# Performance work log

Hardware: AMD Instinct MI355X
Metric: run time of the kernel (lower is better)

Reference implementation:

```python
import jax, jax.numpy as jnp
import numpy as np

H = 768
R = 24


def setup_inputs() -> dict:
    key = jax.random.key(0)
    ks = jax.random.split(key, 9)
    B, S = 4, 256
    hidden = jax.random.normal(ks[0], (B, S, H), dtype=jnp.float32)
    # ConcatHandshaking fc: Linear(2H -> H); torch weight shape (out,in)=(H,2H)
    fc_w = jax.random.normal(ks[1], (H, 2 * H), dtype=jnp.float32) * (1.0 / np.sqrt(2 * H))
    fc_b = jnp.zeros((H,), dtype=jnp.float32)
    # h2t: Linear(H -> 2)
    h2t_w = jax.random.normal(ks[2], (2, H), dtype=jnp.float32) * (1.0 / np.sqrt(H))
    h2t_b = jnp.zeros((2,), dtype=jnp.float32)
    # h2h / t2t TaggingProjector: R independent Linear(H -> 3), batched as (R,3,H)
    h2h_w = jax.random.normal(ks[3], (R, 3, H), dtype=jnp.float32) * (1.0 / np.sqrt(H))
    h2h_b = jnp.zeros((R, 3), dtype=jnp.float32)
    t2t_w = jax.random.normal(ks[4], (R, 3, H), dtype=jnp.float32) * (1.0 / np.sqrt(H))
    t2t_b = jnp.zeros((R, 3), dtype=jnp.float32)
    return {
        "hidden": hidden,
        "fc_w": fc_w, "fc_b": fc_b,
        "h2t_w": h2t_w, "h2t_b": h2t_b,
        "h2h_w": h2h_w, "h2h_b": h2h_b,
        "t2t_w": t2t_w, "t2t_b": t2t_b,
    }


def _handshaking(hidden, fc_w, fc_b):
    # hidden: (B, S, H). Pairs (i, j) with i <= j in row-major (torch loop) order.
    S = hidden.shape[1]
    idx_i, idx_j = jnp.triu_indices(S)  # each (P,), P = S(S+1)/2
    # concat([h_i, h_j]) @ W^T == h_i @ Wl^T + h_j @ Wr^T  (avoids (B,P,2H) buffer)
    Wl = fc_w[:, :H]  # (H, H)
    Wr = fc_w[:, H:]  # (H, H)
    left = jnp.einsum('bsh,oh->bso', hidden, Wl)   # (B, S, H)
    right = jnp.einsum('bsh,oh->bso', hidden, Wr)  # (B, S, H)
    hs = jnp.tanh(left[:, idx_i, :] + right[:, idx_j, :] + fc_b)  # (B, P, H)
    return hs


def reference(hidden, fc_w, fc_b, h2t_w, h2t_b, h2h_w, h2h_b, t2t_w, t2t_b):
    hs = _handshaking(hidden, fc_w, fc_b)  # (B, P, H)
    # h2t: plain Linear(H->2), logits (no softmax in original)
    h2t = jnp.einsum('bph,oh->bpo', hs, h2t_w) + h2t_b  # (B, P, 2)
    # TaggingProjector: batched per-relation Linear(H->3), then softmax over tags
    h2h = jax.nn.softmax(jnp.einsum('bph,rth->brpt', hs, h2h_w) + h2h_b[None, :, None, :], axis=-1)
    t2t = jax.nn.softmax(jnp.einsum('bph,rth->brpt', hs, t2t_w) + t2t_b[None, :, None, :], axis=-1)
    return (h2t, h2h, t2t)
```

## Files before the change

kernel.cpp:

```cpp
#include <hip/hip_runtime.h>
#include <hip/hip_bf16.h>

#define H 768
#define SEQ 256
#define NPAIR 32896
#define NOUTP 160
#define OFF_H2H 263168u
#define OFF_T2T 9737216u

#define N_BPK 122880
#define N_FCW 1179648
#define SCL 2.8853900817779268f

typedef short bf16x8 __attribute__((ext_vector_type(8)));
typedef float f32x4 __attribute__((ext_vector_type(4)));

__device__ __forceinline__ float tanh_s(float xs) {
    float e = __builtin_amdgcn_exp2f(xs);
    return fmaf(-2.0f, __builtin_amdgcn_rcpf(e + 1.0f), 1.0f);
}
__device__ __forceinline__ float bf_lo(int w){ return __uint_as_float(((unsigned)w) << 16); }
__device__ __forceinline__ float bf_hi(int w){ return __uint_as_float(((unsigned)w) & 0xffff0000u); }
__device__ __forceinline__ float bfu(unsigned short u){ return __uint_as_float(((unsigned)u) << 16); }
__device__ __forceinline__ int cvtpk(float lo, float hi) {
    int r;
    asm("v_cvt_pk_bf16_f32 %0, %1, %2" : "=v"(r) : "v"(lo), "v"(hi));
    return r;
}
__device__ __forceinline__ unsigned short bf16r(float x){
    unsigned int u = __float_as_uint(x);
    u += 0x7fffu + ((u >> 16) & 1u);
    return (unsigned short)(u >> 16);
}
__device__ __forceinline__ bf16x8 tanh_frag(int4 lv, int4 rv) {
    int4 st;
    st.x = cvtpk(tanh_s(bf_lo(lv.x) + bf_lo(rv.x)), tanh_s(bf_hi(lv.x) + bf_hi(rv.x)));
    st.y = cvtpk(tanh_s(bf_lo(lv.y) + bf_lo(rv.y)), tanh_s(bf_hi(lv.y) + bf_hi(rv.y)));
    st.z = cvtpk(tanh_s(bf_lo(lv.z) + bf_lo(rv.z)), tanh_s(bf_hi(lv.z) + bf_hi(rv.z)));
    st.w = cvtpk(tanh_s(bf_lo(lv.w) + bf_lo(rv.w)), tanh_s(bf_hi(lv.w) + bf_hi(rv.w)));
    return __builtin_bit_cast(bf16x8, st);
}

typedef const __attribute__((address_space(1))) unsigned int* as1_u32p;
typedef __attribute__((address_space(3))) unsigned int* as3_u32p;
__device__ __forceinline__ void gload_lds16(const void* g, void* l) {
    __builtin_amdgcn_global_load_lds((as1_u32p)g, (as3_u32p)l, 16, 0, 0);
}

__device__ __forceinline__ int row_start(int i) { return i * SEQ - (i * (i - 1)) / 2; }
__device__ __forceinline__ void pair_ij(int p, int& oi, int& oj) {
    double disc = 263169.0 - 8.0 * (double)p;
    int i = (int)((513.0 - sqrt(disc)) * 0.5);
    if (i > 0 && row_start(i) > p) --i;
    while (row_start(i + 1) <= p) ++i;
    oi = i;
    oj = i + (p - row_start(i));
}

__global__ __launch_bounds__(256) void pack_kernel(
    const float* __restrict__ h2t_w, const float* __restrict__ h2h_w,
    const float* __restrict__ t2t_w, const float* __restrict__ h2t_b,
    const float* __restrict__ h2h_b, const float* __restrict__ t2t_b,
    const float* __restrict__ fc_w,
    unsigned short* __restrict__ Bpk, unsigned short* __restrict__ fcwb,
    float* __restrict__ bc)
{
    int idx = blockIdx.x * 256 + threadIdx.x;
    if (idx < N_BPK) {
        int j = idx & 7, lane = (idx >> 3) & 63, rest = idx >> 9;
        int f = rest % 10, k32 = rest / 10;
        int n = f * 16 + (lane & 15);
        int k = k32 * 32 + ((lane >> 4) << 3) + j;
        float v = 0.f;
        if (n < 2)        v = h2t_w[n * H + k];
        else if (n < 74)  v = h2h_w[(n - 2) * H + k];
        else if (n < 146) v = t2t_w[(n - 74) * H + k];
        Bpk[idx] = bf16r(v);
    } else if (idx < N_BPK + N_FCW) {
        int q = idx - N_BPK;
        int n = q / H, k = q % H;
        float v = (n < H) ? fc_w[(size_t)n * 2 * H + k]
                          : fc_w[(size_t)(n - H) * 2 * H + H + k];
        fcwb[q] = bf16r(v);
    } else if (idx < N_BPK + N_FCW + NOUTP) {
        int q = idx - N_BPK - N_FCW;
        float v = 0.f;
        if (q < 2)        v = h2t_b[q];
        else if (q < 74)  v = h2h_b[q - 2];
        else if (q < 146) v = t2t_b[q - 74];
        bc[q] = v;
    }
}

__global__ __launch_bounds__(256, 2) void lr_mfma(
    const float* __restrict__ hidden, const unsigned short* __restrict__ fcwb,
    const float* __restrict__ fc_b,
    unsigned short* __restrict__ LB, unsigned short* __restrict__ RB)
{
    __shared__ __align__(16) char sm[24576];
    const int tid = threadIdx.x, l = tid & 63, w = tid >> 6;
    const int wm = w >> 1, wn = w & 1;
    const int m0 = blockIdx.x * 64, n0 = blockIdx.y * 128;
    f32x4 acc[2][4] = {};
    for (int c = 0; c < 12; ++c) {
        const int k0 = c * 64;
        #pragma unroll
        for (int it = 0; it < 2; ++it) {
            int idx = tid + it * 256;
            int row = idx >> 3, k8 = idx & 7;
            const float4* src = reinterpret_cast<const float4*>(hidden + (size_t)(m0 + row) * H + k0 + k8 * 8);
            float4 a = src[0], bq = src[1];
            int4 st;
            st.x = cvtpk(a.x, a.y);  st.y = cvtpk(a.z, a.w);
            st.z = cvtpk(bq.x, bq.y); st.w = cvtpk(bq.z, bq.w);
            *reinterpret_cast<int4*>(sm + row * 128 + ((k8 * 16) ^ ((row & 7) << 4))) = st;
        }
        #pragma unroll
        for (int it = 0; it < 4; ++it) {
            int idx = tid + it * 256;
            int row = idx >> 3, k8 = idx & 7;
            *reinterpret_cast<int4*>(sm + 8192 + row * 128 + ((k8 * 16) ^ ((row & 7) << 4))) =
                *reinterpret_cast<const int4*>(fcwb + (size_t)(n0 + row) * H + k0 + k8 * 8);
        }
        __syncthreads();
        #pragma unroll
        for (int kk = 0; kk < 2; ++kk) {
            const int sl = kk * 4 + (l >> 4);
            const int swz = (l & 7) << 4;
            bf16x8 af[2], bfr[4];
            #pragma unroll
            for (int a = 0; a < 2; ++a) {
                int row = 32 * wm + 16 * a + (l & 15);
                af[a] = *reinterpret_cast<const bf16x8*>(sm + row * 128 + ((sl * 16) ^ swz));
            }
            #pragma unroll
            for (int f = 0; f < 4; ++f) {
                int row = 64 * wn + 16 * f + (l & 15);
                bfr[f] = *reinterpret_cast<const bf16x8*>(sm + 8192 + row * 128 + ((sl * 16) ^ swz));
            }
            #pragma unroll
            for (int a = 0; a < 2; ++a)
                #pragma unroll
                for (int f = 0; f < 4; ++f)
                    acc[a][f] = __builtin_amdgcn_mfma_f32_16x16x32_bf16(af[a], bfr[f], acc[a][f], 0, 0, 0);
        }
        __syncthreads();
    }
    #pragma unroll
    for (int a = 0; a < 2; ++a)
        #pragma unroll
        for (int f = 0; f < 4; ++f)
            #pragma unroll
            for (int r = 0; r < 4; ++r) {
                int row = m0 + 32 * wm + 16 * a + 4 * (l >> 4) + r;
                int col = n0 + 64 * wn + 16 * f + (l & 15);
                float v = acc[a][f][r];
                if (n0 < H) LB[(size_t)row * H + col] = bf16r((v + fc_b[col]) * SCL);
                else        RB[(size_t)row * H + (col - H)] = bf16r(v * SCL);
            }
}

#define SLAB_STR 166

__global__ __launch_bounds__(256, 3) void pair_mfma(
    const unsigned short* __restrict__ LB, const unsigned short* __restrict__ RB,
    const unsigned short* __restrict__ Bpk, const float* __restrict__ bc,
    float* __restrict__ out)
{
    __shared__ __align__(16) char sm[43136];
    int*   iOf  = reinterpret_cast<int*>(sm);
    int*   jOf  = reinterpret_cast<int*>(sm + 512);
    float* bc_s = reinterpret_cast<float*>(sm + 42496);

    const int tid = threadIdx.x, l = tid & 63, w = tid >> 6;
    const int b = blockIdx.y, p0 = blockIdx.x * 128;

    if (tid < 128) {
        int i, j; pair_ij(p0 + tid, i, j);
        iOf[tid] = i * H; jOf[tid] = j * H;
    }
    if (tid < NOUTP) bc_s[tid] = bc[tid];
    __syncthreads();

    const unsigned short* LBb = LB + (size_t)b * SEQ * H;
    const unsigned short* RBb = RB + (size_t)b * SEQ * H;
    const int row0 = 32 * w + (l & 15);
    const int kb = (l >> 4) << 3;
    const unsigned short* lp0 = LBb + iOf[row0] + kb;
    const unsigned short* rp0 = RBb + jOf[row0] + kb;
    const unsigned short* lp1 = LBb + iOf[row0 + 16] + kb;
    const unsigned short* rp1 = RBb + jOf[row0 + 16] + kb;
    __syncthreads();

    const char* bsrc = reinterpret_cast<const char*>(Bpk) + w * 5120 + l * 16;
    const int ldst_off = w * 5120;

    f32x4 acc[2][10] = {};

    #pragma unroll
    for (int t = 0; t < 5; ++t) gload_lds16(bsrc + t * 1024, sm + ldst_off + t * 1024);
    __builtin_amdgcn_sched_barrier(0);
    int4 lA0 = *reinterpret_cast<const int4*>(lp0);
    int4 lA1 = *reinterpret_cast<const int4*>(lp0 + 32);
    int4 lB0 = *reinterpret_cast<const int4*>(lp1);
    int4 lB1 = *reinterpret_cast<const int4*>(lp1 + 32);
    int4 rA0 = *reinterpret_cast<const int4*>(rp0);
    int4 rA1 = *reinterpret_cast<const int4*>(rp0 + 32);
    int4 rB0 = *reinterpret_cast<const int4*>(rp1);
    int4 rB1 = *reinterpret_cast<const int4*>(rp1 + 32);
    asm volatile("s_waitcnt vmcnt(8) lgkmcnt(0)" ::: "memory");
    __builtin_amdgcn_s_barrier();
    __builtin_amdgcn_sched_barrier(0);

    #pragma unroll 2
    for (int c = 0; c < 11; ++c) {
        char* bufc = sm + ((c & 1) ? 20480 : 0);
        char* bufn = sm + (((c + 1) & 1) ? 20480 : 0);
        const char* bn = bsrc + (c + 1) * 20480;
        #pragma unroll
        for (int t = 0; t < 5; ++t) gload_lds16(bn + t * 1024, bufn + ldst_off + t * 1024);
        __builtin_amdgcn_sched_barrier(0);
        bf16x8 a00 = tanh_frag(lA0, rA0);
        bf16x8 a10 = tanh_frag(lB0, rB0);
        bf16x8 a01 = tanh_frag(lA1, rA1);
        bf16x8 a11 = tanh_frag(lB1, rB1);
        const int co = (c + 1) * 64;
        lA0 = *reinterpret_cast<const int4*>(lp0 + co);
        lA1 = *reinterpret_cast<const int4*>(lp0 + co + 32);
        lB0 = *reinterpret_cast<const int4*>(lp1 + co);
        lB1 = *reinterpret_cast<const int4*>(lp1 + co + 32);
        rA0 = *reinterpret_cast<const int4*>(rp0 + co);
        rA1 = *reinterpret_cast<const int4*>(rp0 + co + 32);
        rB0 = *reinterpret_cast<const int4*>(rp1 + co);
        rB1 = *reinterpret_cast<const int4*>(rp1 + co + 32);
        #pragma unroll
        for (int f = 0; f < 10; ++f) {
            bf16x8 bf0 = *reinterpret_cast<const bf16x8*>(bufc + (f * 64 + l) * 16);
            acc[0][f] = __builtin_amdgcn_mfma_f32_16x16x32_bf16(a00, bf0, acc[0][f], 0, 0, 0);
            acc[1][f] = __builtin_amdgcn_mfma_f32_16x16x32_bf16(a10, bf0, acc[1][f], 0, 0, 0);
        }
        #pragma unroll
        for (int f = 0; f < 10; ++f) {
            bf16x8 bf1 = *reinterpret_cast<const bf16x8*>(bufc + ((10 + f) * 64 + l) * 16);
            acc[0][f] = __builtin_amdgcn_mfma_f32_16x16x32_bf16(a01, bf1, acc[0][f], 0, 0, 0);
            acc[1][f] = __builtin_amdgcn_mfma_f32_16x16x32_bf16(a11, bf1, acc[1][f], 0, 0, 0);
        }
        asm volatile("s_waitcnt vmcnt(8) lgkmcnt(0)" ::: "memory");
        __builtin_amdgcn_s_barrier();
        __builtin_amdgcn_sched_barrier(0);
    }
    {
        bf16x8 a00 = tanh_frag(lA0, rA0);
        bf16x8 a10 = tanh_frag(lB0, rB0);
        bf16x8 a01 = tanh_frag(lA1, rA1);
        bf16x8 a11 = tanh_frag(lB1, rB1);
        const char* bufc = sm + 20480;
        #pragma unroll
        for (int f = 0; f < 10; ++f) {
            bf16x8 bf0 = *reinterpret_cast<const bf16x8*>(bufc + (f * 64 + l) * 16);
            acc[0][f] = __builtin_amdgcn_mfma_f32_16x16x32_bf16(a00, bf0, acc[0][f], 0, 0, 0);
            acc[1][f] = __builtin_amdgcn_mfma_f32_16x16x32_bf16(a10, bf0, acc[1][f], 0, 0, 0);
        }
        #pragma unroll
        for (int f = 0; f < 10; ++f) {
            bf16x8 bf1 = *reinterpret_cast<const bf16x8*>(bufc + ((10 + f) * 64 + l) * 16);
            acc[0][f] = __builtin_amdgcn_mfma_f32_16x16x32_bf16(a01, bf1, acc[0][f], 0, 0, 0);
            acc[1][f] = __builtin_amdgcn_mfma_f32_16x16x32_bf16(a11, bf1, acc[1][f], 0, 0, 0);
        }
    }
    asm volatile("s_waitcnt lgkmcnt(0)" ::: "memory");
    __builtin_amdgcn_s_barrier();

    unsigned short* slab = reinterpret_cast<unsigned short*>(sm);
    #pragma unroll
    for (int m = 0; m < 2; ++m)
        #pragma unroll
        for (int f = 0; f < 10; ++f)
            #pragma unroll
            for (int r = 0; r < 4; ++r) {
                int row = 32 * w + 16 * m + 4 * (l >> 4) + r;
                slab[row * SLAB_STR + f * 16 + (l & 15)] = bf16r(acc[m][f][r]);
            }
    __syncthreads();

    {
        int p = tid >> 1, tt = tid & 1;
        float val = bfu(slab[p * SLAB_STR + tt]) + bc_s[tt];
        __builtin_nontemporal_store(val, &out[((size_t)b * NPAIR + p0 + p) * 2 + tt]);
    }
    #pragma unroll
    for (int it = 0; it < 24; ++it) {
        int item = it * 256 + tid;
        int p = item & 127, rr = item >> 7;
        int ob = 2 + rr * 3;
        const unsigned short* sp = slab + p * SLAB_STR + ob;
        float l0 = bfu(sp[0]) + bc_s[ob + 0];
        float l1 = bfu(sp[1]) + bc_s[ob + 1];
        float l2 = bfu(sp[2]) + bc_s[ob + 2];
        float mx = fmaxf(l0, fmaxf(l1, l2));
        float e0 = __expf(l0 - mx), e1 = __expf(l1 - mx), e2 = __expf(l2 - mx);
        float inv = __fdividef(1.0f, e0 + e1 + e2);
        size_t base = (rr < 24)
            ? (size_t)OFF_H2H + ((size_t)(b * 24 + rr) * NPAIR + p0 + p) * 3
            : (size_t)OFF_T2T + ((size_t)(b * 24 + rr - 24) * NPAIR + p0 + p) * 3;
        __builtin_nontemporal_store(e0 * inv, &out[base + 0]);
        __builtin_nontemporal_store(e1 * inv, &out[base + 1]);
        __builtin_nontemporal_store(e2 * inv, &out[base + 2]);
    }
}

extern "C" void kernel_launch(void* const* d_in, const int* in_sizes, int n_in,
                              void* d_out, int out_size, void* d_ws, size_t ws_size,
                              hipStream_t stream) {
    const float* hidden = (const float*)d_in[0];
    const float* fc_w   = (const float*)d_in[1];
    const float* fc_b   = (const float*)d_in[2];
    const float* h2t_w  = (const float*)d_in[3];
    const float* h2t_b  = (const float*)d_in[4];
    const float* h2h_w  = (const float*)d_in[5];
    const float* h2h_b  = (const float*)d_in[6];
    const float* t2t_w  = (const float*)d_in[7];
    const float* t2t_b  = (const float*)d_in[8];

    char* wsb = (char*)d_ws;
    unsigned short* LBw  = (unsigned short*)(wsb);
    unsigned short* RBw  = (unsigned short*)(wsb + 1572864);
    unsigned short* Bpk  = (unsigned short*)(wsb + 3145728);
    unsigned short* fcwb = (unsigned short*)(wsb + 3391488);
    float*          bc   = (float*)        (wsb + 5750784);

    float* out = (float*)d_out;

    pack_kernel<<<(N_BPK + N_FCW + NOUTP + 255) / 256, 256, 0, stream>>>(
        h2t_w, h2h_w, t2t_w, h2t_b, h2h_b, t2t_b, fc_w, Bpk, fcwb, bc);
    lr_mfma<<<dim3(16, 12), 256, 0, stream>>>(hidden, fcwb, fc_b, LBw, RBw);
    pair_mfma<<<dim3(NPAIR / 128, 4), 256, 0, stream>>>(LBw, RBw, Bpk, bc, out);
}
```

Before: 97.71 us.

## Double pair_mfma block to 256 pairs, flattening batch and pair indices

```diff
diff --git a/kernel.cpp b/kernel.cpp
--- a/kernel.cpp
+++ b/kernel.cpp
@@ -4,6 +4,7 @@
 #define H 768
 #define SEQ 256
 #define NPAIR 32896
+#define NTOT 131584
 #define NOUTP 160
 #define OFF_H2H 263168u
 #define OFF_T2T 9737216u
@@ -55,6 +56,9 @@
     while (row_start(i + 1) <= p) ++i;
     oi = i;
     oj = i + (p - row_start(i));
+}
+__device__ __forceinline__ int batch_of(int g) {
+    return (g >= 3 * NPAIR) ? 3 : (g >= 2 * NPAIR) ? 2 : (g >= NPAIR) ? 1 : 0;
 }
 
 __global__ __launch_bounds__(256) void pack_kernel(
@@ -162,44 +166,49 @@
 
 #define SLAB_STR 166
 
-__global__ __launch_bounds__(256, 3) void pair_mfma(
+__global__ __launch_bounds__(512, 4) void pair_mfma(
     const unsigned short* __restrict__ LB, const unsigned short* __restrict__ RB,
     const unsigned short* __restrict__ Bpk, const float* __restrict__ bc,
     float* __restrict__ out)
 {
     __shared__ __align__(16) char sm[43136];
     int*   iOf  = reinterpret_cast<int*>(sm);
-    int*   jOf  = reinterpret_cast<int*>(sm + 512);
+    int*   jOf  = reinterpret_cast<int*>(sm + 1024);
     float* bc_s = reinterpret_cast<float*>(sm + 42496);
 
     const int tid = threadIdx.x, l = tid & 63, w = tid >> 6;
-    const int b = blockIdx.y, p0 = blockIdx.x * 128;
-
-    if (tid < 128) {
-        int i, j; pair_ij(p0 + tid, i, j);
-        iOf[tid] = i * H; jOf[tid] = j * H;
+    const int g0 = blockIdx.x * 256;
+
+    if (tid < 256) {
+        int g = g0 + tid;
+        int b = batch_of(g);
+        int i, j; pair_ij(g - b * NPAIR, i, j);
+        iOf[tid] = (b * SEQ + i) * H;
+        jOf[tid] = (b * SEQ + j) * H;
     }
     if (tid < NOUTP) bc_s[tid] = bc[tid];
     __syncthreads();
 
-    const unsigned short* LBb = LB + (size_t)b * SEQ * H;
-    const unsigned short* RBb = RB + (size_t)b * SEQ * H;
     const int row0 = 32 * w + (l & 15);
     const int kb = (l >> 4) << 3;
-    const unsigned short* lp0 = LBb + iOf[row0] + kb;
-    const unsigned short* rp0 = RBb + jOf[row0] + kb;
-    const unsigned short* lp1 = LBb + iOf[row0 + 16] + kb;
-    const unsigned short* rp1 = RBb + jOf[row0 + 16] + kb;
+    const unsigned short* lp0 = LB + iOf[row0] + kb;
+    const unsigned short* rp0 = RB + jOf[row0] + kb;
+    const unsigned short* lp1 = LB + iOf[row0 + 16] + kb;
+    const unsigned short* rp1 = RB + jOf[row0 + 16] + kb;
     __syncthreads();
 
-    const char* bsrc = reinterpret_cast<const char*>(Bpk) + w * 5120 + l * 16;
-    const int ldst_off = w * 5120;
+    const char* bpk = reinterpret_cast<const char*>(Bpk);
+    const int ga = 2 * w, gb = 2 * w + 1, gc = 16 + w;
 
     f32x4 acc[2][10] = {};
 
-    #pragma unroll
-    for (int t = 0; t < 5; ++t) gload_lds16(bsrc + t * 1024, sm + ldst_off + t * 1024);
-    __builtin_amdgcn_sched_barrier(0);
+    {
+        const char* bch = bpk;
+        gload_lds16(bch + ga * 1024 + l * 16, sm + ga * 1024);
+        gload_lds16(bch + gb * 1024 + l * 16, sm + gb * 1024);
+        if (w < 4) gload_lds16(bch + gc * 1024 + l * 16, sm + gc * 1024);
+        __builtin_amdgcn_sched_barrier(0);
+    }
     int4 lA0 = *reinterpret_cast<const int4*>(lp0);
     int4 lA1 = *reinterpret_cast<const int4*>(lp0 + 32);
     int4 lB0 = *reinterpret_cast<const int4*>(lp1);
@@ -216,9 +225,10 @@
     for (int c = 0; c < 11; ++c) {
         char* bufc = sm + ((c & 1) ? 20480 : 0);
         char* bufn = sm + (((c + 1) & 1) ? 20480 : 0);
-        const char* bn = bsrc + (c + 1) * 20480;
-        #pragma unroll
-        for (int t = 0; t < 5; ++t) gload_lds16(bn + t * 1024, bufn + ldst_off + t * 1024);
+        const char* bn = bpk + (c + 1) * 20480;
+        gload_lds16(bn + ga * 1024 + l * 16, bufn + ga * 1024);
+        gload_lds16(bn + gb * 1024 + l * 16, bufn + gb * 1024);
+        if (w < 4) gload_lds16(bn + gc * 1024 + l * 16, bufn + gc * 1024);
         __builtin_amdgcn_sched_barrier(0);
         bf16x8 a00 = tanh_frag(lA0, rA0);
         bf16x8 a10 = tanh_frag(lB0, rB0);
@@ -273,39 +283,49 @@
 
     unsigned short* slab = reinterpret_cast<unsigned short*>(sm);
     #pragma unroll
-    for (int m = 0; m < 2; ++m)
-        #pragma unroll
-        for (int f = 0; f < 10; ++f)
-            #pragma unroll
-            for (int r = 0; r < 4; ++r) {
-                int row = 32 * w + 16 * m + 4 * (l >> 4) + r;
-                slab[row * SLAB_STR + f * 16 + (l & 15)] = bf16r(acc[m][f][r]);
-            }
-    __syncthreads();
-
-    {
-        int p = tid >> 1, tt = tid & 1;
-        float val = bfu(slab[p * SLAB_STR + tt]) + bc_s[tt];
-        __builtin_nontemporal_store(val, &out[((size_t)b * NPAIR + p0 + p) * 2 + tt]);
-    }
-    #pragma unroll
-    for (int it = 0; it < 24; ++it) {
-        int item = it * 256 + tid;
-        int p = item & 127, rr = item >> 7;
-        int ob = 2 + rr * 3;
-        const unsigned short* sp = slab + p * SLAB_STR + ob;
-        float l0 = bfu(sp[0]) + bc_s[ob + 0];
-        float l1 = bfu(sp[1]) + bc_s[ob + 1];
-        float l2 = bfu(sp[2]) + bc_s[ob + 2];
-        float mx = fmaxf(l0, fmaxf(l1, l2));
-        float e0 = __expf(l0 - mx), e1 = __expf(l1 - mx), e2 = __expf(l2 - mx);
-        float inv = __fdividef(1.0f, e0 + e1 + e2);
-        size_t base = (rr < 24)
-            ? (size_t)OFF_H2H + ((size_t)(b * 24 + rr) * NPAIR + p0 + p) * 3
-            : (size_t)OFF_T2T + ((size_t)(b * 24 + rr - 24) * NPAIR + p0 + p) * 3;
-        __builtin_nontemporal_store(e0 * inv, &out[base + 0]);
-        __builtin_nontemporal_store(e1 * inv, &out[base + 1]);
-        __builtin_nontemporal_store(e2 * inv, &out[base + 2]);
+    for (int h = 0; h < 2; ++h) {
+        if ((w >> 2) == h) {
+            const int wr = 32 * (w & 3);
+            #pragma unroll
+            for (int m = 0; m < 2; ++m)
+                #pragma unroll
+                for (int f = 0; f < 10; ++f)
+                    #pragma unroll
+                    for (int r = 0; r < 4; ++r) {
+                        int row = wr + 16 * m + 4 * (l >> 4) + r;
+                        slab[row * SLAB_STR + f * 16 + (l & 15)] = bf16r(acc[m][f][r]);
+                    }
+        }
+        __syncthreads();
+        if (tid < 256) {
+            int row = tid >> 1, tt = tid & 1;
+            int g = g0 + 128 * h + row;
+            float val = bfu(slab[row * SLAB_STR + tt]) + bc_s[tt];
+            __builtin_nontemporal_store(val, &out[(size_t)g * 2 + tt]);
+        }
+        #pragma unroll
+        for (int it = 0; it < 12; ++it) {
+            int item = it * 512 + tid;
+            int pr = item & 127, rr = item >> 7;
+            int g = g0 + 128 * h + pr;
+            int b = batch_of(g);
+            int p = g - b * NPAIR;
+            int ob = 2 + rr * 3;
+            const unsigned short* sp = slab + pr * SLAB_STR + ob;
+            float l0 = bfu(sp[0]) + bc_s[ob + 0];
+            float l1 = bfu(sp[1]) + bc_s[ob + 1];
+            float l2 = bfu(sp[2]) + bc_s[ob + 2];
+            float mx = fmaxf(l0, fmaxf(l1, l2));
+            float e0 = __expf(l0 - mx), e1 = __expf(l1 - mx), e2 = __expf(l2 - mx);
+            float inv = __fdividef(1.0f, e0 + e1 + e2);
+            size_t base = (rr < 24)
+                ? (size_t)OFF_H2H + ((size_t)(b * 24 + rr) * NPAIR + p) * 3
+                : (size_t)OFF_T2T + ((size_t)(b * 24 + rr - 24) * NPAIR + p) * 3;
+            __builtin_nontemporal_store(e0 * inv, &out[base + 0]);
+            __builtin_nontemporal_store(e1 * inv, &out[base + 1]);
+            __builtin_nontemporal_store(e2 * inv, &out[base + 2]);
+        }
+        __syncthreads();
     }
 }
 
@@ -334,5 +354,5 @@
     pack_kernel<<<(N_BPK + N_FCW + NOUTP + 255) / 256, 256, 0, stream>>>(
         h2t_w, h2h_w, t2t_w, h2t_b, h2h_b, t2t_b, fc_w, Bpk, fcwb, bc);
     lr_mfma<<<dim3(16, 12), 256, 0, stream>>>(hidden, fcwb, fc_b, LBw, RBw);
-    pair_mfma<<<dim3(NPAIR / 128, 4), 256, 0, stream>>>(LBw, RBw, Bpk, bc, out);
-}
+    pair_mfma<<<514, 512, 0, stream>>>(LBw, RBw, Bpk, bc, out);
+}
```

Result: slower. 149.9 us (+53.4%).

## Shrink pair tile to 64 rows with 32-wide K chunks and flat grid

Applied to the files above, without the earlier changes.

```diff
diff --git a/kernel.cpp b/kernel.cpp
--- a/kernel.cpp
+++ b/kernel.cpp
@@ -4,6 +4,7 @@
 #define H 768
 #define SEQ 256
 #define NPAIR 32896
+#define NTOT 131584
 #define NOUTP 160
 #define OFF_H2H 263168u
 #define OFF_T2T 9737216u
@@ -11,6 +12,11 @@
 #define N_BPK 122880
 #define N_FCW 1179648
 #define SCL 2.8853900817779268f
+
+#define CH 32
+#define NCH 24
+#define BSLOT 12288
+#define SLAB_STR 166
 
 typedef short bf16x8 __attribute__((ext_vector_type(8)));
 typedef float f32x4 __attribute__((ext_vector_type(4)));
@@ -55,6 +61,9 @@
     while (row_start(i + 1) <= p) ++i;
     oi = i;
     oj = i + (p - row_start(i));
+}
+__device__ __forceinline__ int batch_of(int g) {
+    return (g >= 3 * NPAIR) ? 3 : (g >= 2 * NPAIR) ? 2 : (g >= NPAIR) ? 1 : 0;
 }
 
 __global__ __launch_bounds__(256) void pack_kernel(
@@ -68,14 +77,14 @@
     int idx = blockIdx.x * 256 + threadIdx.x;
     if (idx < N_BPK) {
         int j = idx & 7, lane = (idx >> 3) & 63, rest = idx >> 9;
-        int f = rest % 10, k32 = rest / 10;
+        int f = rest % 10, c = rest / 10;
         int n = f * 16 + (lane & 15);
-        int k = k32 * 32 + ((lane >> 4) << 3) + j;
+        int k = c * CH + ((lane >> 4) << 3) + j;
         float v = 0.f;
         if (n < 2)        v = h2t_w[n * H + k];
         else if (n < 74)  v = h2h_w[(n - 2) * H + k];
         else if (n < 146) v = t2t_w[(n - 74) * H + k];
-        Bpk[idx] = bf16r(v);
+        Bpk[c * 6144 + (idx - c * 5120)] = bf16r(v);
     } else if (idx < N_BPK + N_FCW) {
         int q = idx - N_BPK;
         int n = q / H, k = q % H;
@@ -160,112 +169,80 @@
             }
 }
 
-#define SLAB_STR 166
-
-__global__ __launch_bounds__(256, 3) void pair_mfma(
+__global__ __launch_bounds__(256, 4) void pair_mfma(
     const unsigned short* __restrict__ LB, const unsigned short* __restrict__ RB,
     const unsigned short* __restrict__ Bpk, const float* __restrict__ bc,
     float* __restrict__ out)
 {
-    __shared__ __align__(16) char sm[43136];
+    __shared__ __align__(16) char sm[25216];
     int*   iOf  = reinterpret_cast<int*>(sm);
-    int*   jOf  = reinterpret_cast<int*>(sm + 512);
-    float* bc_s = reinterpret_cast<float*>(sm + 42496);
+    int*   jOf  = reinterpret_cast<int*>(sm + 256);
+    float* bc_s = reinterpret_cast<float*>(sm + 24576);
 
     const int tid = threadIdx.x, l = tid & 63, w = tid >> 6;
-    const int b = blockIdx.y, p0 = blockIdx.x * 128;
-
-    if (tid < 128) {
+    const int g0 = blockIdx.x * 64;
+    const int b = batch_of(g0);
+    const int p0 = g0 - b * NPAIR;
+
+    if (tid < 64) {
         int i, j; pair_ij(p0 + tid, i, j);
-        iOf[tid] = i * H; jOf[tid] = j * H;
+        iOf[tid] = (b * SEQ + i) * H;
+        jOf[tid] = (b * SEQ + j) * H;
     }
     if (tid < NOUTP) bc_s[tid] = bc[tid];
     __syncthreads();
 
-    const unsigned short* LBb = LB + (size_t)b * SEQ * H;
-    const unsigned short* RBb = RB + (size_t)b * SEQ * H;
-    const int row0 = 32 * w + (l & 15);
-    const int kb = (l >> 4) << 3;
-    const unsigned short* lp0 = LBb + iOf[row0] + kb;
-    const unsigned short* rp0 = RBb + jOf[row0] + kb;
-    const unsigned short* lp1 = LBb + iOf[row0 + 16] + kb;
-    const unsigned short* rp1 = RBb + jOf[row0 + 16] + kb;
+    const int row = 16 * w + (l & 15);
+    const unsigned short* lp = LB + iOf[row] + ((l >> 4) << 3);
+    const unsigned short* rp = RB + jOf[row] + ((l >> 4) << 3);
     __syncthreads();
 
-    const char* bsrc = reinterpret_cast<const char*>(Bpk) + w * 5120 + l * 16;
-    const int ldst_off = w * 5120;
-
-    f32x4 acc[2][10] = {};
-
-    #pragma unroll
-    for (int t = 0; t < 5; ++t) gload_lds16(bsrc + t * 1024, sm + ldst_off + t * 1024);
-    __builtin_amdgcn_sched_barrier(0);
-    int4 lA0 = *reinterpret_cast<const int4*>(lp0);
-    int4 lA1 = *reinterpret_cast<const int4*>(lp0 + 32);
-    int4 lB0 = *reinterpret_cast<const int4*>(lp1);
-    int4 lB1 = *reinterpret_cast<const int4*>(lp1 + 32);
-    int4 rA0 = *reinterpret_cast<const int4*>(rp0);
-    int4 rA1 = *reinterpret_cast<const int4*>(rp0 + 32);
-    int4 rB0 = *reinterpret_cast<const int4*>(rp1);
-    int4 rB1 = *reinterpret_cast<const int4*>(rp1 + 32);
-    asm volatile("s_waitcnt vmcnt(8) lgkmcnt(0)" ::: "memory");
+    const char* bp = reinterpret_cast<const char*>(Bpk) + w * 1024 + l * 16;
+    const int d0 = w * 1024;
+
+    f32x4 acc[10] = {};
+
+    {
+        gload_lds16(bp,        sm + d0);
+        gload_lds16(bp + 4096, sm + 4096 + d0);
+        gload_lds16(bp + 8192, sm + 8192 + d0);
+        __builtin_amdgcn_sched_barrier(0);
+    }
+    int4 lvC = *reinterpret_cast<const int4*>(lp);
+    int4 rvC = *reinterpret_cast<const int4*>(rp);
+    asm volatile("s_waitcnt vmcnt(2)" ::: "memory");
     __builtin_amdgcn_s_barrier();
     __builtin_amdgcn_sched_barrier(0);
 
-    #pragma unroll 2
-    for (int c = 0; c < 11; ++c) {
-        char* bufc = sm + ((c & 1) ? 20480 : 0);
-        char* bufn = sm + (((c + 1) & 1) ? 20480 : 0);
-        const char* bn = bsrc + (c + 1) * 20480;
-        #pragma unroll
-        for (int t = 0; t < 5; ++t) gload_lds16(bn + t * 1024, bufn + ldst_off + t * 1024);
+    for (int c = 0; c < NCH - 1; ++c) {
+        char* bufn = sm + (((c + 1) & 1) ? BSLOT : 0);
+        const char* bn = bp + (c + 1) * BSLOT;
+        gload_lds16(bn,        bufn + d0);
+        gload_lds16(bn + 4096, bufn + 4096 + d0);
+        gload_lds16(bn + 8192, bufn + 8192 + d0);
         __builtin_amdgcn_sched_barrier(0);
-        bf16x8 a00 = tanh_frag(lA0, rA0);
-        bf16x8 a10 = tanh_frag(lB0, rB0);
-        bf16x8 a01 = tanh_frag(lA1, rA1);
-        bf16x8 a11 = tanh_frag(lB1, rB1);
-        const int co = (c + 1) * 64;
-        lA0 = *reinterpret_cast<const int4*>(lp0 + co);
-        lA1 = *reinterpret_cast<const int4*>(lp0 + co + 32);
-        lB0 = *reinterpret_cast<const int4*>(lp1 + co);
-        lB1 = *reinterpret_cast<const int4*>(lp1 + co + 32);
-        rA0 = *reinterpret_cast<const int4*>(rp0 + co);
-        rA1 = *reinterpret_cast<const int4*>(rp0 + co + 32);
-        rB0 = *reinterpret_cast<const int4*>(rp1 + co);
-        rB1 = *reinterpret_cast<const int4*>(rp1 + co + 32);
+        bf16x8 a0 = tanh_frag(lvC, rvC);
+        const int co = (c + 1) * CH;
+        int4 lvN = *reinterpret_cast<const int4*>(lp + co);
+        int4 rvN = *reinterpret_cast<const int4*>(rp + co);
+        const char* bufc = sm + ((c & 1) ? BSLOT : 0);
         #pragma unroll
         for (int f = 0; f < 10; ++f) {
-            bf16x8 bf0 = *reinterpret_cast<const bf16x8*>(bufc + (f * 64 + l) * 16);
-            acc[0][f] = __builtin_amdgcn_mfma_f32_16x16x32_bf16(a00, bf0, acc[0][f], 0, 0, 0);
-            acc[1][f] = __builtin_amdgcn_mfma_f32_16x16x32_bf16(a10, bf0, acc[1][f], 0, 0, 0);
-        }
-        #pragma unroll
-        for (int f = 0; f < 10; ++f) {
-            bf16x8 bf1 = *reinterpret_cast<const bf16x8*>(bufc + ((10 + f) * 64 + l) * 16);
-            acc[0][f] = __builtin_amdgcn_mfma_f32_16x16x32_bf16(a01, bf1, acc[0][f], 0, 0, 0);
-            acc[1][f] = __builtin_amdgcn_mfma_f32_16x16x32_bf16(a11, bf1, acc[1][f], 0, 0, 0);
-        }
-        asm volatile("s_waitcnt vmcnt(8) lgkmcnt(0)" ::: "memory");
+            bf16x8 bfr = *reinterpret_cast<const bf16x8*>(bufc + (f * 64 + l) * 16);
+            acc[f] = __builtin_amdgcn_mfma_f32_16x16x32_bf16(a0, bfr, acc[f], 0, 0, 0);
+        }
+        asm volatile("s_waitcnt vmcnt(2)" ::: "memory");
         __builtin_amdgcn_s_barrier();
         __builtin_amdgcn_sched_barrier(0);
+        lvC = lvN; rvC = rvN;
     }
     {
-        bf16x8 a00 = tanh_frag(lA0, rA0);
-        bf16x8 a10 = tanh_frag(lB0, rB0);
-        bf16x8 a01 = tanh_frag(lA1, rA1);
-        bf16x8 a11 = tanh_frag(lB1, rB1);
-        const char* bufc = sm + 20480;
+        bf16x8 a0 = tanh_frag(lvC, rvC);
+        const char* bufc = sm + BSLOT;
         #pragma unroll
         for (int f = 0; f < 10; ++f) {
-            bf16x8 bf0 = *reinterpret_cast<const bf16x8*>(bufc + (f * 64 + l) * 16);
-            acc[0][f] = __builtin_amdgcn_mfma_f32_16x16x32_bf16(a00, bf0, acc[0][f], 0, 0, 0);
-            acc[1][f] = __builtin_amdgcn_mfma_f32_16x16x32_bf16(a10, bf0, acc[1][f], 0, 0, 0);
-        }
-        #pragma unroll
-        for (int f = 0; f < 10; ++f) {
-            bf16x8 bf1 = *reinterpret_cast<const bf16x8*>(bufc + ((10 + f) * 64 + l) * 16);
-            acc[0][f] = __builtin_amdgcn_mfma_f32_16x16x32_bf16(a01, bf1, acc[0][f], 0, 0, 0);
-            acc[1][f] = __builtin_amdgcn_mfma_f32_16x16x32_bf16(a11, bf1, acc[1][f], 0, 0, 0);
+            bf16x8 bfr = *reinterpret_cast<const bf16x8*>(bufc + (f * 64 + l) * 16);
+            acc[f] = __builtin_amdgcn_mfma_f32_16x16x32_bf16(a0, bfr, acc[f], 0, 0, 0);
         }
     }
     asm volatile("s_waitcnt lgkmcnt(0)" ::: "memory");
@@ -273,27 +250,26 @@
 
     unsigned short* slab = reinterpret_cast<unsigned short*>(sm);
     #pragma unroll
-    for (int m = 0; m < 2; ++m)
-        #pragma unroll
-        for (int f = 0; f < 10; ++f)
-            #pragma unroll
-            for (int r = 0; r < 4; ++r) {
-                int row = 32 * w + 16 * m + 4 * (l >> 4) + r;
-                slab[row * SLAB_STR + f * 16 + (l & 15)] = bf16r(acc[m][f][r]);
-            }
+    for (int f = 0; f < 10; ++f)
+        #pragma unroll
+        for (int r = 0; r < 4; ++r) {
+            int rw = 16 * w + 4 * (l >> 4) + r;
+            slab[rw * SLAB_STR + f * 16 + (l & 15)] = bf16r(acc[f][r]);
+        }
     __syncthreads();
 
-    {
-        int p = tid >> 1, tt = tid & 1;
-        float val = bfu(slab[p * SLAB_STR + tt]) + bc_s[tt];
-        __builtin_nontemporal_store(val, &out[((size_t)b * NPAIR + p0 + p) * 2 + tt]);
+    if (tid < 128) {
+        int pr = tid >> 1, tt = tid & 1;
+        float val = bfu(slab[pr * SLAB_STR + tt]) + bc_s[tt];
+        __builtin_nontemporal_store(val, &out[(size_t)(g0 + pr) * 2 + tt]);
     }
     #pragma unroll
-    for (int it = 0; it < 24; ++it) {
+    for (int it = 0; it < 12; ++it) {
         int item = it * 256 + tid;
-        int p = item & 127, rr = item >> 7;
+        int pr = item & 63, rr = item >> 6;
+        int p = p0 + pr;
         int ob = 2 + rr * 3;
-        const unsigned short* sp = slab + p * SLAB_STR + ob;
+        const unsigned short* sp = slab + pr * SLAB_STR + ob;
         float l0 = bfu(sp[0]) + bc_s[ob + 0];
         float l1 = bfu(sp[1]) + bc_s[ob + 1];
         float l2 = bfu(sp[2]) + bc_s[ob + 2];
@@ -301,8 +277,8 @@
         float e0 = __expf(l0 - mx), e1 = __expf(l1 - mx), e2 = __expf(l2 - mx);
         float inv = __fdividef(1.0f, e0 + e1 + e2);
         size_t base = (rr < 24)
-            ? (size_t)OFF_H2H + ((size_t)(b * 24 + rr) * NPAIR + p0 + p) * 3
-            : (size_t)OFF_T2T + ((size_t)(b * 24 + rr - 24) * NPAIR + p0 + p) * 3;
+            ? (size_t)OFF_H2H + ((size_t)(b * 24 + rr) * NPAIR + p) * 3
+            : (size_t)OFF_T2T + ((size_t)(b * 24 + rr - 24) * NPAIR + p) * 3;
         __builtin_nontemporal_store(e0 * inv, &out[base + 0]);
         __builtin_nontemporal_store(e1 * inv, &out[base + 1]);
         __builtin_nontemporal_store(e2 * inv, &out[base + 2]);
@@ -326,13 +302,13 @@
     unsigned short* LBw  = (unsigned short*)(wsb);
     unsigned short* RBw  = (unsigned short*)(wsb + 1572864);
     unsigned short* Bpk  = (unsigned short*)(wsb + 3145728);
-    unsigned short* fcwb = (unsigned short*)(wsb + 3391488);
-    float*          bc   = (float*)        (wsb + 5750784);
+    unsigned short* fcwb = (unsigned short*)(wsb + 3440640);
+    float*          bc   = (float*)        (wsb + 5799936);
 
     float* out = (float*)d_out;
 
     pack_kernel<<<(N_BPK + N_FCW + NOUTP + 255) / 256, 256, 0, stream>>>(
         h2t_w, h2h_w, t2t_w, h2t_b, h2h_b, t2t_b, fc_w, Bpk, fcwb, bc);
     lr_mfma<<<dim3(16, 12), 256, 0, stream>>>(hidden, fcwb, fc_b, LBw, RBw);
-    pair_mfma<<<dim3(NPAIR / 128, 4), 256, 0, stream>>>(LBw, RBw, Bpk, bc, out);
-}
+    pair_mfma<<<NTOT / 64, 256, 0, stream>>>(LBw, RBw, Bpk, bc, out);
+}
```

Result: faster. 95.75 us (-2.0%).
